# Kernel optimization log

Measured on AMD Instinct MI355X. Metric: run time of the kernel, lower is better.

Reference implementation:

```python
import jax, jax.numpy as jnp
import numpy as np

B, N, M = 4, 1024, 2048
D, H, HD, L, V = 768, 6, 128, 3, 4096
PEH = 64
FF = 4 * D
TEMP0 = 15.5


def _rms(x, w):
    return x * jax.lax.rsqrt(jnp.mean(x * x, axis=-1, keepdims=True) + 1e-8) * w


def _l2(x):
    n = jnp.sqrt(jnp.sum(x * x, axis=-1, keepdims=True))
    return x / jnp.maximum(n, 1e-12)


def setup_inputs():
    key = jax.random.key(0)
    it = iter(jax.random.split(key, 32))

    def rn(shape, s=0.02):
        return jax.random.normal(next(it), shape, jnp.float32) * s

    inp = {}
    inp['tokens'] = jax.random.randint(next(it), (B, N), 0, V)
    inp['acoustic'] = jax.random.normal(next(it), (B, M, D), jnp.float32)
    inp['embed'] = rn((V, D))
    inp['pe_freq'] = rn((PEH // 2,), 1.0)
    inp['pe_w'] = rn((PEH, D))
    inp['pe_b'] = jnp.zeros((D,), jnp.float32)
    inp['dpb_w0'] = rn((1, 64), 0.5)
    inp['dpb_b0'] = jnp.zeros((64,), jnp.float32)
    inp['dpb_w1'] = rn((64, 64), 0.1)
    inp['dpb_b1'] = jnp.zeros((64,), jnp.float32)
    inp['dpb_w2'] = rn((64, H), 0.1)
    inp['dpb_b2'] = jnp.zeros((H,), jnp.float32)
    inp['acoustic_norm_w'] = jnp.ones((D,), jnp.float32)
    inp['norm1'] = jnp.ones((L, D), jnp.float32)
    inp['norm2'] = jnp.ones((L, D), jnp.float32)
    inp['norm3'] = jnp.ones((L, D), jnp.float32)
    inp['sa_qkv'] = rn((L, D, 3 * H * HD))
    inp['sa_out'] = rn((L, H * HD, D))
    inp['temp'] = jnp.full((L,), TEMP0, jnp.float32)
    inp['ca_q'] = rn((L, D, H * HD))
    inp['ca_kv'] = rn((L, D, 2 * H * HD))
    inp['ca_out'] = rn((L, H * HD, D))
    inp['ff_w1'] = rn((L, D, FF))
    inp['ff_w2'] = rn((L, FF, D))
    inp['final_norm_w'] = jnp.ones((D,), jnp.float32)
    inp['out_w'] = rn((D, V))
    inp['out_b'] = jnp.zeros((V,), jnp.float32)
    return inp


def reference(tokens, acoustic, embed, pe_freq, pe_w, pe_b, dpb_w0, dpb_b0, dpb_w1, dpb_b1, dpb_w2, dpb_b2, acoustic_norm_w, norm1, norm2, norm3, sa_qkv, sa_out, temp, ca_q, ca_kv, ca_out, ff_w1, ff_w2, final_norm_w, out_w, out_b):
    x = embed[tokens]  # [B,N,D]
    # learnable fourier positional encoding (hidden_dim=64)
    p = jnp.arange(N, dtype=jnp.float32)[:, None]
    feat = jnp.concatenate([jnp.cos(p * pe_freq), jnp.sin(p * pe_freq)], axis=-1) / jnp.sqrt(jnp.float32(PEH))
    x = x + (feat @ pe_w + pe_b)

    # DynamicPositionBias: MLP over relative distance -> [H,N,N]
    dist = jnp.arange(-(N - 1), N, dtype=jnp.float32)[:, None]  # [2N-1,1]
    hmlp = jax.nn.silu(dist @ dpb_w0 + dpb_b0)
    hmlp = jax.nn.silu(hmlp @ dpb_w1 + dpb_b1)
    table = hmlp @ dpb_w2 + dpb_b2  # [2N-1, H]
    i = jnp.arange(N)
    rel = i[None, :] - i[:, None] + (N - 1)  # [N,N]
    pos_bias = jnp.transpose(table[rel], (2, 0, 1))  # [H,N,N]
    causal = i[None, :] > i[:, None]  # True where key index > query index
    neg = -jnp.finfo(jnp.float32).max

    xkv = _rms(acoustic, acoustic_norm_w)  # acoustic_norm applied once

    for l in range(L):
        # --- cosine-sim causal self-attention with temperature + pos bias ---
        hx = _rms(x, norm1[l])
        qkv = (hx @ sa_qkv[l]).reshape(B, N, H, HD, 3)  # 'b n (h d qkv)'
        q = jnp.transpose(qkv[..., 0], (0, 2, 1, 3))  # [B,H,N,HD]
        k = jnp.transpose(qkv[..., 1], (0, 2, 1, 3))
        v = jnp.transpose(qkv[..., 2], (0, 2, 1, 3))
        q, k = _l2(q), _l2(k)
        dots = jnp.einsum('bhid,bhjd->bhij', q, k) * temp[l] + pos_bias
        dots = jnp.where(causal, neg, dots)
        attn = jax.nn.softmax(dots, axis=-1)
        o = jnp.einsum('bhij,bhjd->bhid', attn, v)
        o = jnp.transpose(o, (0, 2, 1, 3)).reshape(B, N, H * HD)
        x = x + o @ sa_out[l]

        # --- cross attention to acoustic features (flash-attn math, scale 1/sqrt(d)) ---
        hx = _rms(x, norm2[l])
        q = (hx @ ca_q[l]).reshape(B, N, H, HD)
        kv = (xkv @ ca_kv[l]).reshape(B, M, H, HD, 2)  # 'b n (h d kv)'
        k, v = kv[..., 0], kv[..., 1]
        dots = jnp.einsum('bihd,bjhd->bhij', q, k) / jnp.sqrt(jnp.float32(HD))
        attn = jax.nn.softmax(dots, axis=-1)
        o = jnp.einsum('bhij,bjhd->bihd', attn, v).reshape(B, N, H * HD)
        x = x + o @ ca_out[l]

        # --- feed-forward: linear -> gelu -> linear ---
        hx = _rms(x, norm3[l])
        x = x + jax.nn.gelu(hx @ ff_w1[l], approximate=True) @ ff_w2[l]

    logits = _rms(x, final_norm_w) @ out_w + out_b  # [B,N,V]
    return logits
```

## Files before the change

### kernel.cpp

```cpp
#include <hip/hip_runtime.h>
#include <hip/hip_bf16.h>
#include <math.h>
#include <stddef.h>

#define Bc 4
#define Nc 1024
#define Mc 2048
#define Dc 768
#define Hc 6
#define HDc 128
#define Lc 3
#define Vc 4096
#define FFc 3072

typedef short bf16x8 __attribute__((ext_vector_type(8)));
typedef float f32x4 __attribute__((ext_vector_type(4)));
typedef ushort usx4 __attribute__((ext_vector_type(4)));

__device__ __forceinline__ float gelu_tanh(float x) {
    float x3 = x * x * x;
    return 0.5f * x * (1.0f + tanhf(0.7978845608028654f * (x + 0.044715f * x3)));
}
__device__ __forceinline__ float silu_f(float x) {
    return x / (1.0f + expf(-x));
}
__device__ __forceinline__ ushort f2bf(float x) {
    unsigned u = __float_as_uint(x);
    unsigned r = (u + 0x7fffu + ((u >> 16) & 1u)) >> 16;
    return (ushort)r;
}
__device__ __forceinline__ float bf2f(ushort u) {
    return __uint_as_float(((unsigned)u) << 16);
}
__device__ __forceinline__ void gl2lds16(const ushort* g, ushort* l) {
    __builtin_amdgcn_global_load_lds(
        (const __attribute__((address_space(1))) unsigned int*)(g),
        (__attribute__((address_space(3))) unsigned int*)(l),
        16, 0, 0);
}

__global__ __launch_bounds__(256) void pos_pe_kernel(
    const float* __restrict__ freq, const float* __restrict__ pe_w,
    const float* __restrict__ pe_b, float* __restrict__ pos)
{
    int n = blockIdx.x;
    __shared__ float feat[64];
    int tid = threadIdx.x;
    if (tid < 64) {
        float f;
        if (tid < 32) f = cosf((float)n * freq[tid]);
        else          f = sinf((float)n * freq[tid - 32]);
        feat[tid] = f * 0.125f;
    }
    __syncthreads();
    for (int d = tid; d < Dc; d += 256) {
        float s = pe_b[d];
#pragma unroll
        for (int h = 0; h < 64; ++h) s += feat[h] * pe_w[h * Dc + d];
        pos[(size_t)n * Dc + d] = s;
    }
}

__global__ __launch_bounds__(256) void embed_kernel(
    const int* __restrict__ tokens, const float* __restrict__ embed_w,
    const float* __restrict__ pos, float* __restrict__ x)
{
    size_t idx = (size_t)blockIdx.x * 256 + threadIdx.x;
    if (idx >= (size_t)Bc * Nc * Dc) return;
    int d  = (int)(idx % Dc);
    size_t bn = idx / Dc;
    int n  = (int)(bn % Nc);
    int tok = tokens[bn];
    x[idx] = embed_w[(size_t)tok * Dc + d] + pos[(size_t)n * Dc + d];
}

__global__ __launch_bounds__(64) void dpb_kernel(
    const float* __restrict__ w0, const float* __restrict__ b0,
    const float* __restrict__ w1, const float* __restrict__ b1,
    const float* __restrict__ w2, const float* __restrict__ b2,
    float* __restrict__ table)
{
    int r = blockIdx.x;
    int j = threadIdx.x;
    float dist = (float)r - (float)(Nc - 1);
    __shared__ float s0[64], s1[64];
    s0[j] = silu_f(dist * w0[j] + b0[j]);
    __syncthreads();
    float a = b1[j];
#pragma unroll 8
    for (int k = 0; k < 64; ++k) a += s0[k] * w1[k * 64 + j];
    s1[j] = silu_f(a);
    __syncthreads();
    if (j < Hc) {
        float t = b2[j];
#pragma unroll 8
        for (int k = 0; k < 64; ++k) t += s1[k] * w2[k * Hc + j];
        table[(size_t)r * Hc + j] = t;
    }
}

__global__ __launch_bounds__(256) void rms_kernel(
    const float* __restrict__ in, const float* __restrict__ w,
    ushort* __restrict__ out)
{
    size_t row = blockIdx.x;
    const float* rp = in + row * Dc;
    ushort* op = out + row * Dc;
    int tid = threadIdx.x;
    float s = 0.f;
    for (int d = tid; d < Dc; d += 256) { float v = rp[d]; s += v * v; }
    __shared__ float red[256];
    red[tid] = s;
    __syncthreads();
    for (int o = 128; o > 0; o >>= 1) {
        if (tid < o) red[tid] += red[tid + o];
        __syncthreads();
    }
    float rs = rsqrtf(red[0] * (1.0f / Dc) + 1e-8f);
    for (int d = tid; d < Dc; d += 256) op[d] = f2bf(rp[d] * rs * w[d]);
}

__global__ __launch_bounds__(256) void wt_kernel(
    const float* __restrict__ in, ushort* __restrict__ out, int K_, int N_)
{
    int n0 = blockIdx.x << 6, k0 = blockIdx.y << 6;
    __shared__ ushort t[64][65];
    int tid = threadIdx.x;
    int r = tid >> 4, c4 = (tid & 15) << 2;
    for (int rr = r; rr < 64; rr += 16) {
        float4 v = *(const float4*)&in[(size_t)(k0 + rr) * N_ + n0 + c4];
        t[rr][c4]     = f2bf(v.x);
        t[rr][c4 + 1] = f2bf(v.y);
        t[rr][c4 + 2] = f2bf(v.z);
        t[rr][c4 + 3] = f2bf(v.w);
    }
    __syncthreads();
    int nr = tid >> 2, cw = (tid & 3) << 4;
    ushort tmp[16];
#pragma unroll
    for (int j = 0; j < 16; ++j) tmp[j] = t[cw + j][nr];
#pragma unroll
    for (int s = 0; s < 2; ++s)
        *(bf16x8*)&out[(size_t)(n0 + nr) * K_ + k0 + cw + (s << 3)] =
            *(const bf16x8*)&tmp[s << 3];
}

__global__ __launch_bounds__(256) void gemm_bf16_kernel(
    const ushort* __restrict__ A, const ushort* __restrict__ Bt,
    const float* __restrict__ bias, const float* __restrict__ res,
    float* __restrict__ Cf, ushort* __restrict__ Cb,
    int M_, int N_, int K_, int act, int ksplit)
{
    __shared__ __align__(16) ushort As[2][8 * 512];
    __shared__ __align__(16) ushort Bs[2][8 * 512];
    int m0 = blockIdx.y << 7, n0 = blockIdx.x << 7;
    int tid = threadIdx.x;
    int wave = tid >> 6, lane = tid & 63;
    int li = lane & 15, lq = lane >> 4;
    int wm = (wave >> 1) << 6, wn = (wave & 1) << 6;

    int kchunk = K_ / ksplit;
    int kbeg = blockIdx.z * kchunk;
    int niter = kchunk >> 5;

    f32x4 acc[4][4];
#pragma unroll
    for (int i = 0; i < 4; ++i)
#pragma unroll
        for (int j = 0; j < 4; ++j) {
            acc[i][j][0] = 0.f; acc[i][j][1] = 0.f;
            acc[i][j][2] = 0.f; acc[i][j][3] = 0.f;
        }

    auto stage = [&](int buf, int k0) {
#pragma unroll
        for (int i = 0; i < 2; ++i) {
            int fb = (wave << 1) + i;
            const ushort* ga = A  + (size_t)(m0 + (fb << 4) + li) * K_ + k0 + (lq << 3);
            const ushort* gb = Bt + (size_t)(n0 + (fb << 4) + li) * K_ + k0 + (lq << 3);
            gl2lds16(ga, &As[buf][fb << 9]);
            gl2lds16(gb, &Bs[buf][fb << 9]);
        }
    };

    stage(0, kbeg);
    __syncthreads();

    for (int it = 0; it < niter; ++it) {
        int cur = it & 1;
        if (it + 1 < niter) stage(cur ^ 1, kbeg + ((it + 1) << 5));
        bf16x8 af[4], bfr[4];
#pragma unroll
        for (int t = 0; t < 4; ++t) {
            af[t]  = *(const bf16x8*)&As[cur][(((wm >> 4) + t) << 9) + (lane << 3)];
            bfr[t] = *(const bf16x8*)&Bs[cur][(((wn >> 4) + t) << 9) + (lane << 3)];
        }
#pragma unroll
        for (int mt = 0; mt < 4; ++mt)
#pragma unroll
            for (int nt = 0; nt < 4; ++nt)
                acc[mt][nt] = __builtin_amdgcn_mfma_f32_16x16x32_bf16(
                    af[mt], bfr[nt], acc[mt][nt], 0, 0, 0);
        __syncthreads();
    }

    if (ksplit > 1) {
#pragma unroll
        for (int mt = 0; mt < 4; ++mt) {
#pragma unroll
            for (int r = 0; r < 4; ++r) {
                int row = m0 + wm + (mt << 4) + (lq << 2) + r;
#pragma unroll
                for (int nt = 0; nt < 4; ++nt) {
                    int col = n0 + wn + (nt << 4) + li;
                    atomicAdd(&Cf[(size_t)row * N_ + col], acc[mt][nt][r]);
                }
            }
        }
        return;
    }

#pragma unroll
    for (int mt = 0; mt < 4; ++mt) {
#pragma unroll
        for (int r = 0; r < 4; ++r) {
            int row = m0 + wm + (mt << 4) + (lq << 2) + r;
#pragma unroll
            for (int nt = 0; nt < 4; ++nt) {
                int col = n0 + wn + (nt << 4) + li;
                float v = acc[mt][nt][r];
                if (bias) v += bias[col];
                if (act == 1) v = gelu_tanh(v);
                if (res) v += res[(size_t)row * N_ + col];
                if (Cb) Cb[(size_t)row * N_ + col] = f2bf(v);
                else    Cf[(size_t)row * N_ + col] = v;
            }
        }
    }
}

__global__ __launch_bounds__(128) void unpack_sa_kernel(
    const ushort* __restrict__ qkv, ushort* __restrict__ qo,
    ushort* __restrict__ ko, ushort* __restrict__ vo)
{
    int bid = blockIdx.x;
    int h = bid % Hc;
    int bn = bid / Hc;
    int b = bn / Nc, n = bn % Nc;
    int d = threadIdx.x;
    size_t base = (size_t)bn * (3 * Hc * HDc) + (size_t)(h * HDc + d) * 3;
    float q = bf2f(qkv[base]), k = bf2f(qkv[base + 1]);
    ushort v = qkv[base + 2];
    __shared__ float rq[128], rk[128];
    rq[d] = q * q; rk[d] = k * k;
    __syncthreads();
    for (int o = 64; o > 0; o >>= 1) {
        if (d < o) { rq[d] += rq[d + o]; rk[d] += rk[d + o]; }
        __syncthreads();
    }
    float qn = fmaxf(sqrtf(rq[0]), 1e-12f);
    float kn = fmaxf(sqrtf(rk[0]), 1e-12f);
    size_t oidx = (((size_t)(b * Hc + h) * Nc) + n) * HDc + d;
    qo[oidx] = f2bf(q / qn);
    ko[oidx] = f2bf(k / kn);
    vo[oidx] = v;
}

__global__ __launch_bounds__(256) void unpack_caq_kernel(
    const ushort* __restrict__ in, ushort* __restrict__ qo)
{
    size_t idx = (size_t)blockIdx.x * 256 + threadIdx.x;
    if (idx >= (size_t)Bc * Hc * Nc * HDc) return;
    int d = (int)(idx & (HDc - 1));
    size_t t = idx >> 7;
    int n = (int)(t % Nc); t /= Nc;
    int h = (int)(t % Hc); int b = (int)(t / Hc);
    qo[idx] = in[((size_t)(b * Nc + n)) * (Hc * HDc) + h * HDc + d];
}

__global__ __launch_bounds__(256) void unpack_cakv_kernel(
    const ushort* __restrict__ in, ushort* __restrict__ ko, ushort* __restrict__ vo)
{
    size_t idx = (size_t)blockIdx.x * 256 + threadIdx.x;
    if (idx >= (size_t)Bc * Hc * Mc * HDc) return;
    int d = (int)(idx & (HDc - 1));
    size_t t = idx >> 7;
    int m = (int)(t % Mc); t /= Mc;
    int h = (int)(t % Hc); int b = (int)(t / Hc);
    size_t src = ((size_t)(b * Mc + m)) * (2 * Hc * HDc) + (size_t)(h * HDc + d) * 2;
    ko[idx] = in[src];
    vo[idx] = in[src + 1];
}

__global__ __launch_bounds__(256) void transpose_kernel(
    const ushort* __restrict__ in, ushort* __restrict__ out, int R)
{
    int bh = blockIdx.z;
    int r0 = blockIdx.x << 6, d0 = blockIdx.y << 6;
    const ushort* ip = in + (size_t)bh * R * HDc;
    ushort* op = out + (size_t)bh * HDc * R;
    __shared__ ushort tile[64][66];
    int t = threadIdx.x;
    int lr = t >> 5, lc = (t & 31) << 1;
    for (int rr = lr; rr < 64; rr += 8) {
        ushort2 v = *(const ushort2*)&ip[(size_t)(r0 + rr) * HDc + d0 + lc];
        tile[rr][lc] = v.x; tile[rr][lc + 1] = v.y;
    }
    __syncthreads();
    for (int dd = lr; dd < 64; dd += 8) {
        ushort2 v;
        v.x = tile[lc][dd]; v.y = tile[lc + 1][dd];
        *(ushort2*)&op[(size_t)(d0 + dd) * R + r0 + lc] = v;
    }
}

__global__ __launch_bounds__(256) void attn_mfma_kernel(
    const ushort* __restrict__ Qg, const ushort* __restrict__ Kg,
    const ushort* __restrict__ VTg, ushort* __restrict__ O,
    int NQ, int NK, float scale_const, const float* __restrict__ scale_ptr,
    const float* __restrict__ bias_table, int causal)
{
    int qtiles = NQ >> 6;
    int qt = blockIdx.x % qtiles;
    int bh = blockIdx.x / qtiles;
    int h = bh % Hc, b = bh / Hc;
    int q0 = qt << 6;

    const ushort* Qb = Qg + (size_t)bh * NQ * HDc;
    const ushort* Kb = Kg + (size_t)bh * NK * HDc;
    const ushort* Vb = VTg + (size_t)bh * HDc * NK;

    float scale = scale_const * (scale_ptr ? scale_ptr[0] : 1.0f);

    __shared__ __align__(16) ushort Ks[2][16 * 512];
    __shared__ __align__(16) ushort Vs[2][16 * 512];
    __shared__ __align__(16) ushort Ps[4][16][72];
    __shared__ float bias_s[2][128];

    int tid = threadIdx.x;
    int wave = tid >> 6, lane = tid & 63;
    int li = lane & 15, lq = lane >> 4;
    int qrel = (wave << 4) + li;

    bf16x8 qfrag[4];
    {
        const ushort* qrow = Qb + (size_t)(q0 + qrel) * HDc + (lq << 3);
#pragma unroll
        for (int kt = 0; kt < 4; ++kt)
            qfrag[kt] = *(const bf16x8*)&qrow[kt << 5];
    }

    f32x4 oacc[8];
#pragma unroll
    for (int i = 0; i < 8; ++i) { oacc[i][0] = 0.f; oacc[i][1] = 0.f; oacc[i][2] = 0.f; oacc[i][3] = 0.f; }
    float m_run = -INFINITY, l_run = 0.f;

    auto stage_kv = [&](int buf, int jt) {
        int j0 = jt << 6;
#pragma unroll
        for (int i = 0; i < 4; ++i) {
            int f = (wave << 2) + i;
            int mt = f >> 2, kt = f & 3;
            const ushort* gk = Kb + (size_t)(j0 + (mt << 4) + li) * HDc + (kt << 5) + (lq << 3);
            gl2lds16(gk, &Ks[buf][f << 9]);
            int dt = f >> 1, s = f & 1;
            const ushort* gv = Vb + (size_t)((dt << 4) + li) * NK + j0 + (s << 5) + (lq << 3);
            gl2lds16(gv, &Vs[buf][f << 9]);
        }
        if (bias_table && tid < 127)
            bias_s[buf][tid] = bias_table[(size_t)(j0 - q0 - 63 + Nc - 1 + tid) * Hc + h];
    };

    int jt_end = causal ? (q0 >> 6) + 1 : (NK >> 6);

    stage_kv(0, 0);
    __syncthreads();

    for (int jt = 0; jt < jt_end; ++jt) {
        int cur = jt & 1;
        if (jt + 1 < jt_end) stage_kv(cur ^ 1, jt + 1);
        int j0 = jt << 6;

        f32x4 sacc[4];
#pragma unroll
        for (int mt = 0; mt < 4; ++mt) {
            f32x4 s; s[0] = 0.f; s[1] = 0.f; s[2] = 0.f; s[3] = 0.f;
#pragma unroll
            for (int kt = 0; kt < 4; ++kt) {
                bf16x8 kf = *(const bf16x8*)&Ks[cur][(((mt << 2) + kt) << 9) + (lane << 3)];
                s = __builtin_amdgcn_mfma_f32_16x16x32_bf16(kf, qfrag[kt], s, 0, 0, 0);
            }
            sacc[mt] = s;
        }

        float sv[4][4];
        float mtile = -INFINITY;
#pragma unroll
        for (int mt = 0; mt < 4; ++mt)
#pragma unroll
            for (int r = 0; r < 4; ++r) {
                int jrel = (mt << 4) + (lq << 2) + r;
                float sx = sacc[mt][r] * scale;
                if (bias_table) sx += bias_s[cur][jrel - qrel + 63];
                if (causal && (j0 + jrel) > (q0 + qrel)) sx = -INFINITY;
                sv[mt][r] = sx;
                mtile = fmaxf(mtile, sx);
            }
        mtile = fmaxf(mtile, __shfl_xor(mtile, 16));
        mtile = fmaxf(mtile, __shfl_xor(mtile, 32));
        float m_new = fmaxf(m_run, mtile);
        float alpha = __expf(m_run - m_new);
        m_run = m_new;
        float ps = 0.f;
#pragma unroll
        for (int mt = 0; mt < 4; ++mt)
#pragma unroll
            for (int r = 0; r < 4; ++r) {
                float p = __expf(sv[mt][r] - m_new);
                sv[mt][r] = p;
                ps += p;
            }
        ps += __shfl_xor(ps, 16);
        ps += __shfl_xor(ps, 32);
        l_run = l_run * alpha + ps;

#pragma unroll
        for (int mt = 0; mt < 4; ++mt) {
            usx4 pk;
            pk.x = f2bf(sv[mt][0]); pk.y = f2bf(sv[mt][1]);
            pk.z = f2bf(sv[mt][2]); pk.w = f2bf(sv[mt][3]);
            *(usx4*)&Ps[wave][li][(mt << 4) + (lq << 2)] = pk;
        }

        float ar[4];
#pragma unroll
        for (int r = 0; r < 4; ++r) ar[r] = __shfl(alpha, (lq << 2) + r);
#pragma unroll
        for (int dt = 0; dt < 8; ++dt)
#pragma unroll
            for (int r = 0; r < 4; ++r) oacc[dt][r] *= ar[r];

        bf16x8 pf0 = *(const bf16x8*)&Ps[wave][li][(lq << 3)];
        bf16x8 pf1 = *(const bf16x8*)&Ps[wave][li][32 + (lq << 3)];
#pragma unroll
        for (int dt = 0; dt < 8; ++dt) {
            bf16x8 v0 = *(const bf16x8*)&Vs[cur][(((dt << 1) + 0) << 9) + (lane << 3)];
            bf16x8 v1 = *(const bf16x8*)&Vs[cur][(((dt << 1) + 1) << 9) + (lane << 3)];
            oacc[dt] = __builtin_amdgcn_mfma_f32_16x16x32_bf16(pf0, v0, oacc[dt], 0, 0, 0);
            oacc[dt] = __builtin_amdgcn_mfma_f32_16x16x32_bf16(pf1, v1, oacc[dt], 0, 0, 0);
        }
        __syncthreads();
    }

#pragma unroll
    for (int r = 0; r < 4; ++r) {
        float linv = 1.0f / __shfl(l_run, (lq << 2) + r);
        int gq = q0 + (wave << 4) + (lq << 2) + r;
        ushort* op = O + ((size_t)(b * NQ + gq)) * (Hc * HDc) + h * HDc;
#pragma unroll
        for (int dt = 0; dt < 8; ++dt)
            op[(dt << 4) + li] = f2bf(oacc[dt][r] * linv);
    }
}

static inline void launch_gemm(const ushort* A, const ushort* Bt, const float* bias,
                               const float* res, float* Cf, ushort* Cb,
                               int M_, int N_, int K_, int act, int ksplit,
                               hipStream_t s)
{
    dim3 g(N_ / 128, M_ / 128, ksplit);
    hipLaunchKernelGGL(gemm_bf16_kernel, g, dim3(256), 0, s,
                       A, Bt, bias, res, Cf, Cb, M_, N_, K_, act, ksplit);
}

extern "C" void kernel_launch(void* const* d_in, const int* in_sizes, int n_in,
                              void* d_out, int out_size, void* d_ws, size_t ws_size,
                              hipStream_t stream)
{
    const int*   tokens   = (const int*)  d_in[0];
    const float* acoustic = (const float*)d_in[1];
    const float* embed_w  = (const float*)d_in[2];
    const float* pe_freq  = (const float*)d_in[3];
    const float* pe_w     = (const float*)d_in[4];
    const float* pe_b     = (const float*)d_in[5];
    const float* dpb_w0   = (const float*)d_in[6];
    const float* dpb_b0   = (const float*)d_in[7];
    const float* dpb_w1   = (const float*)d_in[8];
    const float* dpb_b1   = (const float*)d_in[9];
    const float* dpb_w2   = (const float*)d_in[10];
    const float* dpb_b2   = (const float*)d_in[11];
    const float* ac_nw    = (const float*)d_in[12];
    const float* norm1    = (const float*)d_in[13];
    const float* norm2    = (const float*)d_in[14];
    const float* norm3    = (const float*)d_in[15];
    const float* sa_qkv   = (const float*)d_in[16];
    const float* sa_out_w = (const float*)d_in[17];
    const float* temp     = (const float*)d_in[18];
    const float* ca_q_w   = (const float*)d_in[19];
    const float* ca_kv_w  = (const float*)d_in[20];
    const float* ca_out_w = (const float*)d_in[21];
    const float* ff_w1    = (const float*)d_in[22];
    const float* ff_w2    = (const float*)d_in[23];
    const float* fin_nw   = (const float*)d_in[24];
    const float* out_w    = (const float*)d_in[25];
    const float* out_b    = (const float*)d_in[26];
    float* out = (float*)d_out;

    const size_t SZ_X   = (size_t)Bc * Nc * Dc;
    const size_t SZ_POS = (size_t)Nc * Dc;
    const size_t SZ_TAB = 16384;
    const size_t SZ_XKV = (size_t)Bc * Mc * Dc;
    const size_t SZ_BIG = (size_t)Bc * Nc * FFc;
    const size_t SZ_QH  = (size_t)Bc * Hc * Nc * HDc;
    const size_t SZ_KH  = (size_t)Bc * Hc * Mc * HDc;

    float* ws = (float*)d_ws;
    float* x     = ws;
    float* pos   = x + SZ_X;
    float* table = pos + SZ_POS;
    ushort* hx    = (ushort*)(table + SZ_TAB);
    ushort* xkvb  = hx + SZ_X;
    ushort* attnO = xkvb + SZ_XKV;
    ushort* bigBb = attnO + SZ_X;
    ushort* qb    = bigBb + SZ_BIG;
    ushort* kb    = qb + SZ_QH;
    ushort* vb    = kb + SZ_KH;
    ushort* vTb   = vb + SZ_KH;
    ushort* wT    = vTb + SZ_KH;

    const size_t W_QKV = (size_t)Dc * 3 * Hc * HDc;
    const size_t W_O   = (size_t)Hc * HDc * Dc;
    const size_t W_CKV = (size_t)Dc * 2 * Hc * HDc;
    const size_t W_F   = (size_t)Dc * FFc;
    const size_t W_LAYER = W_QKV + 3 * W_O + W_CKV + 2 * W_F;
    ushort* outWT = wT + 3 * W_LAYER;

    const float CA_SCALE = 0.08838834764831843f;

    for (int l = 0; l < Lc; ++l) {
        ushort* wl = wT + (size_t)l * W_LAYER;
        ushort* qkvT = wl;
        ushort* soT  = qkvT + W_QKV;
        ushort* cqT  = soT + W_O;
        ushort* ckvT = cqT + W_O;
        ushort* coT  = ckvT + W_CKV;
        ushort* f1T  = coT + W_O;
        ushort* f2T  = f1T + W_F;
        hipLaunchKernelGGL(wt_kernel, dim3(3 * Hc * HDc / 64, Dc / 64), dim3(256), 0, stream,
                           sa_qkv + (size_t)l * W_QKV, qkvT, Dc, 3 * Hc * HDc);
        hipLaunchKernelGGL(wt_kernel, dim3(Dc / 64, Hc * HDc / 64), dim3(256), 0, stream,
                           sa_out_w + (size_t)l * W_O, soT, Hc * HDc, Dc);
        hipLaunchKernelGGL(wt_kernel, dim3(Hc * HDc / 64, Dc / 64), dim3(256), 0, stream,
                           ca_q_w + (size_t)l * W_O, cqT, Dc, Hc * HDc);
        hipLaunchKernelGGL(wt_kernel, dim3(2 * Hc * HDc / 64, Dc / 64), dim3(256), 0, stream,
                           ca_kv_w + (size_t)l * W_CKV, ckvT, Dc, 2 * Hc * HDc);
        hipLaunchKernelGGL(wt_kernel, dim3(Dc / 64, Hc * HDc / 64), dim3(256), 0, stream,
                           ca_out_w + (size_t)l * W_O, coT, Hc * HDc, Dc);
        hipLaunchKernelGGL(wt_kernel, dim3(FFc / 64, Dc / 64), dim3(256), 0, stream,
                           ff_w1 + (size_t)l * W_F, f1T, Dc, FFc);
        hipLaunchKernelGGL(wt_kernel, dim3(Dc / 64, FFc / 64), dim3(256), 0, stream,
                           ff_w2 + (size_t)l * W_F, f2T, FFc, Dc);
    }
    hipLaunchKernelGGL(wt_kernel, dim3(Vc / 64, Dc / 64), dim3(256), 0, stream,
                       out_w, outWT, Dc, Vc);

    hipLaunchKernelGGL(pos_pe_kernel, dim3(Nc), dim3(256), 0, stream,
                       pe_freq, pe_w, pe_b, pos);
    hipLaunchKernelGGL(embed_kernel, dim3((unsigned)((SZ_X + 255) / 256)), dim3(256), 0, stream,
                       tokens, embed_w, pos, x);
    hipLaunchKernelGGL(dpb_kernel, dim3(2 * Nc - 1), dim3(64), 0, stream,
                       dpb_w0, dpb_b0, dpb_w1, dpb_b1, dpb_w2, dpb_b2, table);
    hipLaunchKernelGGL(rms_kernel, dim3(Bc * Mc), dim3(256), 0, stream,
                       acoustic, ac_nw, xkvb);

    for (int l = 0; l < Lc; ++l) {
        const float* n1 = norm1 + (size_t)l * Dc;
        const float* n2 = norm2 + (size_t)l * Dc;
        const float* n3 = norm3 + (size_t)l * Dc;
        ushort* wl = wT + (size_t)l * W_LAYER;
        ushort* qkvT = wl;
        ushort* soT  = qkvT + W_QKV;
        ushort* cqT  = soT + W_O;
        ushort* ckvT = cqT + W_O;
        ushort* coT  = ckvT + W_CKV;
        ushort* f1T  = coT + W_O;
        ushort* f2T  = f1T + W_F;

        hipLaunchKernelGGL(rms_kernel, dim3(Bc * Nc), dim3(256), 0, stream, x, n1, hx);
        launch_gemm(hx, qkvT, nullptr, nullptr, nullptr, bigBb,
                    Bc * Nc, 3 * Hc * HDc, Dc, 0, 1, stream);
        hipLaunchKernelGGL(unpack_sa_kernel, dim3(Bc * Nc * Hc), dim3(128), 0, stream,
                           bigBb, qb, kb, vb);
        hipLaunchKernelGGL(transpose_kernel, dim3(Nc / 64, 2, Bc * Hc), dim3(256), 0, stream,
                           vb, vTb, Nc);
        hipLaunchKernelGGL(attn_mfma_kernel, dim3(Bc * Hc * (Nc / 64)), dim3(256), 0, stream,
                           qb, kb, vTb, attnO, Nc, Nc, 1.0f, temp + l, table, 1);
        launch_gemm(attnO, soT, nullptr, nullptr, x, nullptr,
                    Bc * Nc, Dc, Hc * HDc, 0, 2, stream);

        hipLaunchKernelGGL(rms_kernel, dim3(Bc * Nc), dim3(256), 0, stream, x, n2, hx);
        launch_gemm(hx, cqT, nullptr, nullptr, nullptr, bigBb,
                    Bc * Nc, Hc * HDc, Dc, 0, 1, stream);
        hipLaunchKernelGGL(unpack_caq_kernel, dim3((unsigned)((SZ_QH + 255) / 256)), dim3(256),
                           0, stream, bigBb, qb);
        launch_gemm(xkvb, ckvT, nullptr, nullptr, nullptr, bigBb,
                    Bc * Mc, 2 * Hc * HDc, Dc, 0, 1, stream);
        hipLaunchKernelGGL(unpack_cakv_kernel, dim3((unsigned)((SZ_KH + 255) / 256)), dim3(256),
                           0, stream, bigBb, kb, vb);
        hipLaunchKernelGGL(transpose_kernel, dim3(Mc / 64, 2, Bc * Hc), dim3(256), 0, stream,
                           vb, vTb, Mc);
        hipLaunchKernelGGL(attn_mfma_kernel, dim3(Bc * Hc * (Nc / 64)), dim3(256), 0, stream,
                           qb, kb, vTb, attnO, Nc, Mc, CA_SCALE, nullptr, nullptr, 0);
        launch_gemm(attnO, coT, nullptr, nullptr, x, nullptr,
                    Bc * Nc, Dc, Hc * HDc, 0, 2, stream);

        hipLaunchKernelGGL(rms_kernel, dim3(Bc * Nc), dim3(256), 0, stream, x, n3, hx);
        launch_gemm(hx, f1T, nullptr, nullptr, nullptr, bigBb,
                    Bc * Nc, FFc, Dc, 1, 1, stream);
        launch_gemm(bigBb, f2T, nullptr, nullptr, x, nullptr,
                    Bc * Nc, Dc, FFc, 0, 4, stream);
    }

    hipLaunchKernelGGL(rms_kernel, dim3(Bc * Nc), dim3(256), 0, stream, x, fin_nw, hx);
    launch_gemm(hx, outWT, out_b, nullptr, out, nullptr,
                Bc * Nc, Vc, Dc, 0, 1, stream);
}
```

Measured before the change: 1.940 ms.

## Replace split-K atomics with partial buffers reduced inside fused RMSNorm

Split-K GEMMs now write their partial sums to separate fp32 slabs instead of using atomicAdd on the residual. The following RMSNorm kernel sums the partials into the residual stream and normalises in the same pass. The cross-attention Q projection now uses split-K with its reduction folded into the unpack kernel. The goal is to remove atomic contention and extra passes over the residual. The cost is extra fp32 traffic for the partial buffers, which alias the q/k scratch buffers, and split factors that change from 2 or 4 to 3.

```diff
diff --git a/kernel.cpp b/kernel.cpp
--- a/kernel.cpp
+++ b/kernel.cpp
@@ -118,6 +118,40 @@
     }
     float rs = rsqrtf(red[0] * (1.0f / Dc) + 1e-8f);
     for (int d = tid; d < Dc; d += 256) op[d] = f2bf(rp[d] * rs * w[d]);
+}
+
+__global__ __launch_bounds__(256) void rms_reduce_kernel(
+    float* __restrict__ x, const float* __restrict__ P, int nsplit, size_t MN,
+    const float* __restrict__ w, ushort* __restrict__ out)
+{
+    size_t row = blockIdx.x;
+    float* xp = x + row * Dc;
+    ushort* op = out + row * Dc;
+    int tid = threadIdx.x;
+    float v[3];
+    float s = 0.f;
+#pragma unroll
+    for (int i = 0; i < 3; ++i) {
+        int d = tid + (i << 8);
+        float t = xp[d];
+        for (int z = 0; z < nsplit; ++z) t += P[(size_t)z * MN + row * Dc + d];
+        xp[d] = t;
+        v[i] = t;
+        s += t * t;
+    }
+    __shared__ float red[256];
+    red[tid] = s;
+    __syncthreads();
+    for (int o = 128; o > 0; o >>= 1) {
+        if (tid < o) red[tid] += red[tid + o];
+        __syncthreads();
+    }
+    float rs = rsqrtf(red[0] * (1.0f / Dc) + 1e-8f);
+#pragma unroll
+    for (int i = 0; i < 3; ++i) {
+        int d = tid + (i << 8);
+        op[d] = f2bf(v[i] * rs * w[d]);
+    }
 }
 
 __global__ __launch_bounds__(256) void wt_kernel(
@@ -205,6 +239,7 @@
     }
 
     if (ksplit > 1) {
+        float* Pz = Cf + (size_t)blockIdx.z * M_ * N_;
 #pragma unroll
         for (int mt = 0; mt < 4; ++mt) {
 #pragma unroll
@@ -213,7 +248,7 @@
 #pragma unroll
                 for (int nt = 0; nt < 4; ++nt) {
                     int col = n0 + wn + (nt << 4) + li;
-                    atomicAdd(&Cf[(size_t)row * N_ + col], acc[mt][nt][r]);
+                    Pz[(size_t)row * N_ + col] = acc[mt][nt][r];
                 }
             }
         }
@@ -266,8 +301,8 @@
     vo[oidx] = v;
 }
 
-__global__ __launch_bounds__(256) void unpack_caq_kernel(
-    const ushort* __restrict__ in, ushort* __restrict__ qo)
+__global__ __launch_bounds__(256) void unpack_caq_red_kernel(
+    const float* __restrict__ P, ushort* __restrict__ qo)
 {
     size_t idx = (size_t)blockIdx.x * 256 + threadIdx.x;
     if (idx >= (size_t)Bc * Hc * Nc * HDc) return;
@@ -275,7 +310,9 @@
     size_t t = idx >> 7;
     int n = (int)(t % Nc); t /= Nc;
     int h = (int)(t % Hc); int b = (int)(t / Hc);
-    qo[idx] = in[((size_t)(b * Nc + n)) * (Hc * HDc) + h * HDc + d];
+    const size_t MNq = (size_t)Bc * Nc * (Hc * HDc);
+    size_t src = ((size_t)(b * Nc + n)) * (Hc * HDc) + h * HDc + d;
+    qo[idx] = f2bf(P[src] + P[MNq + src]);
 }
 
 __global__ __launch_bounds__(256) void unpack_cakv_kernel(
@@ -535,6 +572,10 @@
     const size_t W_LAYER = W_QKV + 3 * W_O + W_CKV + 2 * W_F;
     ushort* outWT = wT + 3 * W_LAYER;
 
+    float* Pq = (float*)qb;
+    float* Pk = (float*)kb;
+    const size_t MN = (size_t)Bc * Nc * Dc;
+
     const float CA_SCALE = 0.08838834764831843f;
 
     for (int l = 0; l < Lc; ++l) {
@@ -586,7 +627,11 @@
         ushort* f1T  = coT + W_O;
         ushort* f2T  = f1T + W_F;
 
-        hipLaunchKernelGGL(rms_kernel, dim3(Bc * Nc), dim3(256), 0, stream, x, n1, hx);
+        if (l == 0)
+            hipLaunchKernelGGL(rms_kernel, dim3(Bc * Nc), dim3(256), 0, stream, x, n1, hx);
+        else
+            hipLaunchKernelGGL(rms_reduce_kernel, dim3(Bc * Nc), dim3(256), 0, stream,
+                               x, Pq, 3, MN, n1, hx);
         launch_gemm(hx, qkvT, nullptr, nullptr, nullptr, bigBb,
                     Bc * Nc, 3 * Hc * HDc, Dc, 0, 1, stream);
         hipLaunchKernelGGL(unpack_sa_kernel, dim3(Bc * Nc * Hc), dim3(128), 0, stream,
@@ -595,14 +640,15 @@
                            vb, vTb, Nc);
         hipLaunchKernelGGL(attn_mfma_kernel, dim3(Bc * Hc * (Nc / 64)), dim3(256), 0, stream,
                            qb, kb, vTb, attnO, Nc, Nc, 1.0f, temp + l, table, 1);
-        launch_gemm(attnO, soT, nullptr, nullptr, x, nullptr,
-                    Bc * Nc, Dc, Hc * HDc, 0, 2, stream);
-
-        hipLaunchKernelGGL(rms_kernel, dim3(Bc * Nc), dim3(256), 0, stream, x, n2, hx);
-        launch_gemm(hx, cqT, nullptr, nullptr, nullptr, bigBb,
-                    Bc * Nc, Hc * HDc, Dc, 0, 1, stream);
-        hipLaunchKernelGGL(unpack_caq_kernel, dim3((unsigned)((SZ_QH + 255) / 256)), dim3(256),
-                           0, stream, bigBb, qb);
+        launch_gemm(attnO, soT, nullptr, nullptr, Pq, nullptr,
+                    Bc * Nc, Dc, Hc * HDc, 0, 3, stream);
+        hipLaunchKernelGGL(rms_reduce_kernel, dim3(Bc * Nc), dim3(256), 0, stream,
+                           x, Pq, 3, MN, n2, hx);
+
+        launch_gemm(hx, cqT, nullptr, nullptr, Pk, nullptr,
+                    Bc * Nc, Hc * HDc, Dc, 0, 2, stream);
+        hipLaunchKernelGGL(unpack_caq_red_kernel, dim3((unsigned)((SZ_QH + 255) / 256)),
+                           dim3(256), 0, stream, Pk, qb);
         launch_gemm(xkvb, ckvT, nullptr, nullptr, nullptr, bigBb,
                     Bc * Mc, 2 * Hc * HDc, Dc, 0, 1, stream);
         hipLaunchKernelGGL(unpack_cakv_kernel, dim3((unsigned)((SZ_KH + 255) / 256)), dim3(256),
@@ -611,17 +657,19 @@
                            vb, vTb, Mc);
         hipLaunchKernelGGL(attn_mfma_kernel, dim3(Bc * Hc * (Nc / 64)), dim3(256), 0, stream,
                            qb, kb, vTb, attnO, Nc, Mc, CA_SCALE, nullptr, nullptr, 0);
-        launch_gemm(attnO, coT, nullptr, nullptr, x, nullptr,
-                    Bc * Nc, Dc, Hc * HDc, 0, 2, stream);
-
-        hipLaunchKernelGGL(rms_kernel, dim3(Bc * Nc), dim3(256), 0, stream, x, n3, hx);
+        launch_gemm(attnO, coT, nullptr, nullptr, Pq, nullptr,
+                    Bc * Nc, Dc, Hc * HDc, 0, 3, stream);
+        hipLaunchKernelGGL(rms_reduce_kernel, dim3(Bc * Nc), dim3(256), 0, stream,
+                           x, Pq, 3, MN, n3, hx);
+
         launch_gemm(hx, f1T, nullptr, nullptr, nullptr, bigBb,
                     Bc * Nc, FFc, Dc, 1, 1, stream);
-        launch_gemm(bigBb, f2T, nullptr, nullptr, x, nullptr,
-                    Bc * Nc, Dc, FFc, 0, 4, stream);
-    }
-
-    hipLaunchKernelGGL(rms_kernel, dim3(Bc * Nc), dim3(256), 0, stream, x, fin_nw, hx);
+        launch_gemm(bigBb, f2T, nullptr, nullptr, Pq, nullptr,
+                    Bc * Nc, Dc, FFc, 0, 3, stream);
+    }
+
+    hipLaunchKernelGGL(rms_reduce_kernel, dim3(Bc * Nc), dim3(256), 0, stream,
+                       x, Pq, 3, MN, fin_nw, hx);
     launch_gemm(hx, outWT, out_b, nullptr, out, nullptr,
                 Bc * Nc, Vc, Dc, 0, 1, stream);
 }
```

New measurement: 1.826 ms. 1.06x faster.
